# Kernel optimization log

Measured on AMD Instinct MI355X. Metric: run time of the kernel, lower is better.

Reference implementation:

```python
import jax, jax.numpy as jnp
import numpy as np

DIM = 768
HEADS = 12
HEAD_DIM = DIM // HEADS
GRID = 32
MLP_HIDDEN = DIM * 4
EPS = 1e-5


def layernorm(x, g, b):
    m = jnp.mean(x, axis=-1, keepdims=True)
    v = jnp.mean((x - m) ** 2, axis=-1, keepdims=True)
    return (x - m) * jax.lax.rsqrt(v + EPS) * g + b


def geometry_bias(wg_w, wg_b):
    # Box-relational embedding on a GRIDxGRID grid; batch-invariant so computed once.
    g = GRID
    idx = jnp.arange(g, dtype=jnp.float32)
    px = jnp.repeat(idx, g) / g          # row index, normalized
    py = jnp.tile(idx, g) / g            # col index, normalized
    cx = px + 0.5 / g
    cy = py + 0.5 / g
    wbox = 1.0 + 1.0 / g                 # x_max - x_min + 1 (constant)
    dx = jnp.log(jnp.clip(jnp.abs((cx[:, None] - cx[None, :]) / wbox), 1e-3, None))
    dy = jnp.log(jnp.clip(jnp.abs((cy[:, None] - cy[None, :]) / wbox), 1e-3, None))
    dz = jnp.zeros_like(dx)              # log(w/w) = log(h/h) = 0
    pos = jnp.stack([dx, dy, dz, dz], axis=-1)                      # [N,N,4]
    dim_mat = 1.0 / (1000.0 ** (jnp.arange(8, dtype=jnp.float32) / 8.0))
    mul = (100.0 * pos)[..., None] * dim_mat                        # [N,N,4,8]
    mul = mul.reshape(g * g, g * g, 32)
    emb = jnp.concatenate([jnp.sin(mul), jnp.cos(mul)], axis=-1)    # [N,N,64]
    w = jax.nn.relu(jnp.einsum('ijd,hd->hij', emb, wg_w) + wg_b[:, None, None])
    rgw = jnp.log(jnp.clip(w, 1e-6, None))                          # [H,N,N]
    return jnp.pad(rgw, ((0, 0), (1, 0), (1, 0)))                   # zero row/col for cls


def mha(x, qkv_w, proj_w, proj_b, bias=None):
    Bt, N, C = x.shape
    qkv = (x @ qkv_w.T).reshape(Bt, N, 3, HEADS, HEAD_DIM).transpose(2, 0, 3, 1, 4)
    q, k, v = qkv[0], qkv[1], qkv[2]
    attn = jnp.einsum('bhid,bhjd->bhij', q, k) * (HEAD_DIM ** -0.5)
    if bias is not None:
        attn = attn + bias
    attn = jax.nn.softmax(attn, axis=-1)
    out = jnp.einsum('bhij,bhjd->bhid', attn, v).transpose(0, 2, 1, 3).reshape(Bt, N, C)
    return out @ proj_w.T + proj_b


def mlp(x, fc1_w, fc1_b, fc2_w, fc2_b):
    h = jax.nn.gelu(x @ fc1_w.T + fc1_b, approximate=False)
    return h @ fc2_w.T + fc2_b


def setup_inputs() -> dict:
    key = jax.random.key(0)
    ks = jax.random.split(key, 16)
    s = 0.02
    d = {
        'x': jax.random.normal(ks[0], (2, 4097, DIM), dtype=jnp.float32),
        'norm1_g': jnp.ones((DIM,), jnp.float32), 'norm1_b': jnp.zeros((DIM,), jnp.float32),
        'qkv_w': s * jax.random.normal(ks[1], (3 * DIM, DIM), dtype=jnp.float32),
        'proj_w': s * jax.random.normal(ks[2], (DIM, DIM), dtype=jnp.float32),
        'proj_b': jnp.zeros((DIM,), jnp.float32),
        'wg_w': s * jax.random.normal(ks[3], (HEADS, 64), dtype=jnp.float32),
        'wg_b': s * jax.random.normal(ks[4], (HEADS,), dtype=jnp.float32),
        'tnorm1_g': jnp.ones((DIM,), jnp.float32), 'tnorm1_b': jnp.zeros((DIM,), jnp.float32),
        'tqkv_w': s * jax.random.normal(ks[5], (3 * DIM, DIM), dtype=jnp.float32),
        'tproj_w': s * jax.random.normal(ks[6], (DIM, DIM), dtype=jnp.float32),
        'tproj_b': jnp.zeros((DIM,), jnp.float32),
        'tfc_w': s * jax.random.normal(ks[7], (DIM, DIM), dtype=jnp.float32),
        'tfc_b': jnp.zeros((DIM,), jnp.float32),
        'norm2_g': jnp.ones((DIM,), jnp.float32), 'norm2_b': jnp.zeros((DIM,), jnp.float32),
        'fc1_w': s * jax.random.normal(ks[8], (MLP_HIDDEN, DIM), dtype=jnp.float32),
        'fc1_b': jnp.zeros((MLP_HIDDEN,), jnp.float32),
        'fc2_w': s * jax.random.normal(ks[9], (DIM, MLP_HIDDEN), dtype=jnp.float32),
        'fc2_b': jnp.zeros((DIM,), jnp.float32),
        'B': 2, 'T': 4, 'W': 32,
    }
    return d


def reference(x, norm1_g, norm1_b, qkv_w, proj_w, proj_b, wg_w, wg_b,
              tnorm1_g, tnorm1_b, tqkv_w, tproj_w, tproj_b, tfc_w, tfc_b,
              norm2_g, norm2_b, fc1_w, fc1_b, fc2_w, fc2_b, B, T, W):
    m = x.shape[2]
    H = ((x.shape[1] - 1) // T) // W
    # temporal attention: b (h w t) m -> (b h w) t m
    xt = x[:, 1:, :]
    xt_t = xt.reshape(B, H, W, T, m).reshape(B * H * W, T, m)
    res_t = mha(layernorm(xt_t, tnorm1_g, tnorm1_b), tqkv_w, tproj_w, tproj_b)
    res_t = res_t.reshape(B, H, W, T, m).reshape(B, H * W * T, m)
    res_t = res_t @ tfc_w.T + tfc_b
    xt = x[:, 1:, :] + res_t
    # spatial attention with geometric bias: b (h w t) m -> (b t) (h w) m
    init_cls = x[:, 0:1, :]
    cls = jnp.broadcast_to(init_cls, (B, T, m)).reshape(B * T, 1, m)
    xs = xt.reshape(B, H, W, T, m).transpose(0, 3, 1, 2, 4).reshape(B * T, H * W, m)
    xs = jnp.concatenate([cls, xs], axis=1)
    bias = geometry_bias(wg_w, wg_b)[None]  # [1,heads,1+HW,1+HW]
    res_s = mha(layernorm(xs, norm1_g, norm1_b), qkv_w, proj_w, proj_b, bias=bias)
    cls_out = res_s[:, 0, :].reshape(B, T, m).mean(axis=1, keepdims=True)
    res_s = res_s[:, 1:, :].reshape(B, T, H, W, m).transpose(0, 2, 3, 1, 4).reshape(B, H * W * T, m)
    xout = jnp.concatenate([init_cls, xt], axis=1) + jnp.concatenate([cls_out, res_s], axis=1)
    xout = xout + mlp(layernorm(xout, norm2_g, norm2_b), fc1_w, fc1_b, fc2_w, fc2_b)
    return xout
```

## Files before the change

### kernel.cpp

```cpp
#include <hip/hip_runtime.h>
#include <stdint.h>

#define DIM   768
#define HEADS 12
#define NSP   1025
#define VT_LD 1152
#define PS_LD 72

typedef __attribute__((ext_vector_type(8))) short short8;
typedef __attribute__((ext_vector_type(4))) float f32x4;
typedef unsigned short u16;
typedef unsigned int   u32;

__device__ __forceinline__ u16 f2bf(float v) {
  u32 u = __builtin_bit_cast(u32, v);
  u += 0x7fffu + ((u >> 16) & 1u);
  return (u16)(u >> 16);
}
__device__ __forceinline__ float bf2f(u16 h) {
  u32 u = ((u32)h) << 16;
  return __builtin_bit_cast(float, u);
}

__device__ __forceinline__ void load_lds16(const u16* g, u16* lbase, int lane) {
#if __has_builtin(__builtin_amdgcn_global_load_lds)
  __builtin_amdgcn_global_load_lds((const __attribute__((address_space(1))) void*)g,
                                   (__attribute__((address_space(3))) void*)lbase, 16, 0, 0);
#else
  *(short8*)(lbase + lane * 8) = *(const short8*)g;
#endif
}

__global__ __launch_bounds__(256) void zero_k(float* __restrict__ o, long n) {
  long i = (long)blockIdx.x * 256 + threadIdx.x;
  if (i < n) o[i] = 0.0f;
}

__global__ __launch_bounds__(256) void cvt_k(const float* __restrict__ src,
                                             u16* __restrict__ dst, long n) {
  long i = (long)blockIdx.x * 256 + threadIdx.x;
  if (i < n) dst[i] = f2bf(src[i]);
}

__device__ __forceinline__ void ln_row(const float* __restrict__ src,
                                       u16* __restrict__ dst,
                                       const float* __restrict__ g,
                                       const float* __restrict__ b) {
  int tid = threadIdx.x;
  float v[3];
  float s = 0.f, ss = 0.f;
#pragma unroll
  for (int i = 0; i < 3; i++) {
    v[i] = src[tid + i * 256];
    s += v[i];
    ss += v[i] * v[i];
  }
  __shared__ float red[8];
#pragma unroll
  for (int m = 32; m; m >>= 1) {
    s  += __shfl_xor(s, m);
    ss += __shfl_xor(ss, m);
  }
  int wid = tid >> 6;
  if ((tid & 63) == 0) { red[wid] = s; red[4 + wid] = ss; }
  __syncthreads();
  s  = red[0] + red[1] + red[2] + red[3];
  ss = red[4] + red[5] + red[6] + red[7];
  float mean = s * (1.0f / 768.0f);
  float var  = ss * (1.0f / 768.0f) - mean * mean;
  float rs = rsqrtf(var + 1e-5f);
#pragma unroll
  for (int i = 0; i < 3; i++) {
    int c = tid + i * 256;
    dst[c] = f2bf((v[i] - mean) * rs * g[c] + b[c]);
  }
}

__global__ __launch_bounds__(256) void ln_xt_k(const float* __restrict__ x,
                                               const float* __restrict__ g,
                                               const float* __restrict__ b,
                                               u16* __restrict__ outb) {
  int q = blockIdx.x, bb = blockIdx.y;
  const float* src = x + ((long)bb * 4097 + 1 + q) * DIM;
  u16* dst = outb + ((long)bb * 4096 + q) * DIM;
  ln_row(src, dst, g, b);
}

__global__ __launch_bounds__(256) void ln_xs_k(const float* __restrict__ x,
                                               const float* __restrict__ xt,
                                               const float* __restrict__ g,
                                               const float* __restrict__ b,
                                               u16* __restrict__ outb) {
  int n = blockIdx.x, bt = blockIdx.y;
  int bb = bt >> 2, t = bt & 3;
  const float* src;
  if (n == 0) src = x + (long)bb * 4097 * DIM;
  else        src = xt + ((long)bb * 4096 + (long)(n - 1) * 4 + t) * DIM;
  u16* dst = outb + ((long)bt * NSP + n) * DIM;
  ln_row(src, dst, g, b);
}

struct GemmParams {
  const u16* A; long lda, sA1;
  const u16* B; long ldb;
  void* C;      long ldc, sC1;
  const float* bias;
  const float* resid; long ldr, sR1;
  float scale;
  int M, N, K;
};

template <bool OUTBF16, bool BIASV, bool RESID, bool GELU_, bool NT64>
__global__ __launch_bounds__(256) void gemm_k(GemmParams p) {
  constexpr int NJ = NT64 ? 2 : 4;
  __shared__ u16 As[4096];
  __shared__ u16 Bs[NT64 ? 2048 : 4096];
  int tid = threadIdx.x;
  int z1 = blockIdx.z;
  const u16* A = p.A + (long)z1 * p.sA1;
  const u16* B = p.B;
  int m0 = blockIdx.y * 128, n0 = blockIdx.x * (NT64 ? 64 : 128);
  int wave = tid >> 6, lane = tid & 63;
  int quad = lane >> 4, lrow = lane & 15;
  int wm = (wave & 1) * 64;
  int wn = NT64 ? (wave >> 1) * 32 : (wave >> 1) * 64;

  int rA0 = m0 + (tid >> 2);        if (rA0 > p.M - 1) rA0 = p.M - 1;
  int rA1 = m0 + 64 + (tid >> 2);   if (rA1 > p.M - 1) rA1 = p.M - 1;
  int c8 = (tid & 3) << 3;
  const u16* pa0 = A + (long)rA0 * p.lda + c8;
  const u16* pa1 = A + (long)rA1 * p.lda + c8;
  u16* lA0 = As + wave * 512;  u16* lA1 = As + 2048 + wave * 512;

  const u16 *pb0, *pb1 = nullptr;
  u16 *lB0, *lB1 = nullptr;
  {
    int rB0 = n0 + (tid >> 2);
    if (!NT64) {
      int rB1 = n0 + 64 + (tid >> 2);
      if (rB0 > p.N - 1) rB0 = p.N - 1;
      if (rB1 > p.N - 1) rB1 = p.N - 1;
      pb1 = B + (long)rB1 * p.ldb + c8;
      lB1 = Bs + 2048 + wave * 512;
    }
    pb0 = B + (long)rB0 * p.ldb + c8;
    lB0 = Bs + wave * 512;
  }

  f32x4 acc[4][NJ];
#pragma unroll
  for (int i = 0; i < 4; i++)
#pragma unroll
    for (int j = 0; j < NJ; j++) acc[i][j] = (f32x4){0.f, 0.f, 0.f, 0.f};

  for (int k0 = 0; k0 < p.K; k0 += 32) {
    load_lds16(pa0 + k0, lA0, lane);
    load_lds16(pa1 + k0, lA1, lane);
    load_lds16(pb0 + k0, lB0, lane);
    if (!NT64) load_lds16(pb1 + k0, lB1, lane);
    __syncthreads();
    short8 af[4], bfr[NJ];
#pragma unroll
    for (int i = 0; i < 4; i++)  af[i]  = *(const short8*)&As[(wm + i * 16 + lrow) * 32 + quad * 8];
#pragma unroll
    for (int j = 0; j < NJ; j++) bfr[j] = *(const short8*)&Bs[(wn + j * 16 + lrow) * 32 + quad * 8];
#pragma unroll
    for (int i = 0; i < 4; i++)
#pragma unroll
      for (int j = 0; j < NJ; j++)
        acc[i][j] = __builtin_amdgcn_mfma_f32_16x16x32_bf16(af[i], bfr[j], acc[i][j], 0, 0, 0);
    __syncthreads();
  }

  float* Cf = (float*)p.C;
  u16*   Ch = (u16*)p.C;
  long cbase = (long)z1 * p.sC1;
#pragma unroll
  for (int i = 0; i < 4; i++) {
    int rbase = m0 + wm + i * 16 + quad * 4;
#pragma unroll
    for (int j = 0; j < NJ; j++) {
      int c = n0 + wn + j * 16 + lrow;
      if (c >= p.N) continue;
#pragma unroll
      for (int rr = 0; rr < 4; rr++) {
        int r = rbase + rr;
        if (r >= p.M) continue;
        float v = acc[i][j][rr] * p.scale;
        if (BIASV) v += p.bias[c];
        if (GELU_) v = 0.5f * v * (1.0f + erff(v * 0.70710678118654752f));
        if (RESID) v += p.resid[(long)z1 * p.sR1 + (long)r * p.ldr + c];
        long o = cbase + (long)r * p.ldc + c;
        if (OUTBF16) Ch[o] = f2bf(v);
        else         Cf[o] = v;
      }
    }
  }
}

__global__ __launch_bounds__(64) void attn_t_k(const u16* __restrict__ qkv,
                                               u16* __restrict__ outb) {
  int h = blockIdx.x;
  int g = blockIdx.y;
  int d = threadIdx.x;
  long base = (long)g * 4 * 2304 + h * 64 + d;
  float q[4], k[4], vv[4];
#pragma unroll
  for (int t = 0; t < 4; t++) {
    q[t]  = bf2f(qkv[base + (long)t * 2304]);
    k[t]  = bf2f(qkv[base + (long)t * 2304 + 768]);
    vv[t] = bf2f(qkv[base + (long)t * 2304 + 1536]);
  }
  float sc[4][4];
#pragma unroll
  for (int i = 0; i < 4; i++)
#pragma unroll
    for (int j = 0; j < 4; j++) {
      float pv = q[i] * k[j];
#pragma unroll
      for (int m = 32; m; m >>= 1) pv += __shfl_xor(pv, m);
      sc[i][j] = pv * 0.125f;
    }
#pragma unroll
  for (int i = 0; i < 4; i++) {
    float mx = fmaxf(fmaxf(sc[i][0], sc[i][1]), fmaxf(sc[i][2], sc[i][3]));
    float e0 = __expf(sc[i][0] - mx), e1 = __expf(sc[i][1] - mx);
    float e2 = __expf(sc[i][2] - mx), e3 = __expf(sc[i][3] - mx);
    float inv = 1.0f / (e0 + e1 + e2 + e3);
    float ov = (e0 * vv[0] + e1 * vv[1] + e2 * vv[2] + e3 * vv[3]) * inv;
    outb[((long)g * 4 + i) * DIM + h * 64 + d] = f2bf(ov);
  }
}

__global__ void geo_pre_k(const float* __restrict__ wg_w,
                          const float* __restrict__ wg_b,
                          float* __restrict__ sxsyc) {
  int t = threadIdx.x;
  if (t >= 384) return;
  int h = t >> 5, dd = t & 31;
  float dx = logf(fmaxf((float)dd * (1.0f / 33.0f), 0.001f));
  float sx = 0.f, sy = 0.f;
#pragma unroll
  for (int k2 = 0; k2 < 8; k2++) {
    float dm = powf(1000.0f, -(float)k2 / 8.0f);
    float a = 100.0f * dx * dm;
    float sn = sinf(a), cs = cosf(a);
    sx += sn * wg_w[h * 64 + k2]     + cs * wg_w[h * 64 + 32 + k2];
    sy += sn * wg_w[h * 64 + 8 + k2] + cs * wg_w[h * 64 + 40 + k2];
  }
  sxsyc[t] = sx;
  sxsyc[384 + t] = sy;
  if (dd == 0) {
    float c = wg_b[h];
#pragma unroll
    for (int k2 = 48; k2 < 64; k2++) c += wg_w[h * 64 + k2];
    sxsyc[768 + h] = c;
  }
}

__global__ __launch_bounds__(256) void geo_bias_k(const float* __restrict__ sxsyc,
                                                  float* __restrict__ Bh_g) {
  int h = blockIdx.x / 4;
  int idx = (blockIdx.x % 4) * 256 + threadIdx.x;
  int dr = idx >> 5, dc = idx & 31;
  float v = sxsyc[h * 32 + dr] + sxsyc[384 + h * 32 + dc] + sxsyc[768 + h];
  Bh_g[h * 1024 + idx] = logf(fmaxf(fmaxf(v, 0.0f), 1e-6f));
}

__global__ __launch_bounds__(256) void vtrans_k(const u16* __restrict__ qkv_s,
                                                u16* __restrict__ Vt) {
  __shared__ u16 tile[64][33];
  int bh = blockIdx.y;
  int bt = bh / 12, h = bh % 12;
  int j0 = blockIdx.x * 32;
  int tid = threadIdx.x;
#pragma unroll
  for (int it = 0; it < 8; it++) {
    int jj = it * 4 + (tid >> 6);
    int d = tid & 63;
    int j = j0 + jj;
    u16 v = 0;
    if (j < NSP) v = qkv_s[((long)bt * NSP + j) * 2304 + 1536 + h * 64 + d];
    tile[d][jj] = v;
  }
  __syncthreads();
#pragma unroll
  for (int it = 0; it < 8; it++) {
    int d = it * 8 + (tid >> 5);
    int j = tid & 31;
    Vt[((long)bh * 64 + d) * VT_LD + j0 + j] = tile[d][j];
  }
}

__global__ __launch_bounds__(256, 4) void attn_s_k(const u16* __restrict__ qkv,
                                                   const u16* __restrict__ Vt,
                                                   const float* __restrict__ Bh_g,
                                                   u16* __restrict__ attn_o) {
  __shared__ u16 KsF[8192];
  __shared__ u16 UN[4608];
  __shared__ float BhS[1024];
  const int bid = blockIdx.x;
  const int slot = bid >> 3;
  const int bh = (bid & 7) * 12 + slot / 17;
  const int qt = slot % 17;
  const int bt = bh / 12, h = bh % 12;
  const int tid = threadIdx.x;
  const int wave = tid >> 6, lane = tid & 63;
  const int quad = lane >> 4, lr = lane & 15;
  const int m0 = qt * 64;
  const long qb = (long)bt * NSP * 2304 + h * 64;

#pragma unroll
  for (int i = 0; i < 4; i++) BhS[tid + i * 256] = Bh_g[h * 1024 + tid + i * 256];

  const int rowq = tid >> 2, colq = (tid & 3) << 3;
  {
    int tokq = m0 + rowq; if (tokq > 1024) tokq = 1024;
    const u16* gq = qkv + qb + (long)tokq * 2304 + colq;
    load_lds16(gq,      UN + wave * 512, lane);
    load_lds16(gq + 32, UN + 2048 + wave * 512, lane);
  }
  {
    int t0 = rowq; if (t0 > 1024) t0 = 1024;
    const u16* g0 = qkv + qb + 768 + (long)t0 * 2304 + colq;
    load_lds16(g0,      KsF + wave * 512, lane);
    load_lds16(g0 + 32, KsF + 2048 + wave * 512, lane);
  }
  __syncthreads();
  short8 qf[2];
#pragma unroll
  for (int ks = 0; ks < 2; ks++)
    qf[ks] = *(const short8*)&UN[ks * 2048 + (wave * 16 + lr) * 32 + quad * 8];

  f32x4 Oa[4];
  float mr[4], lsum[4];
#pragma unroll
  for (int n = 0; n < 4; n++) Oa[n] = (f32x4){0.f, 0.f, 0.f, 0.f};
#pragma unroll
  for (int r = 0; r < 4; r++) { mr[r] = -1e30f; lsum[r] = 0.f; }

  int rid[4], ri_[4], ci_[4];
  float rok[4];
#pragma unroll
  for (int r = 0; r < 4; r++) {
    int i0 = m0 + wave * 16 + quad * 4 + r;
    rid[r] = i0;
    int ii = i0 < NSP ? i0 : (NSP - 1);
    int im1 = ii > 0 ? ii - 1 : 0;
    ri_[r] = im1 >> 5;
    ci_[r] = im1 & 31;
    rok[r] = (i0 > 0) ? 1.0f : 0.0f;
  }

  const u16* vrow = Vt + ((long)bh * 64 + lr) * VT_LD;

  for (int kt = 0; kt < 17; kt++) {
    const int cur = kt & 1, nxt = cur ^ 1;
    if (kt < 16) {
      int t0 = (kt + 1) * 64 + rowq; if (t0 > 1024) t0 = 1024;
      const u16* g0 = qkv + qb + 768 + (long)t0 * 2304 + colq;
      load_lds16(g0,      KsF + nxt * 4096 + wave * 512, lane);
      load_lds16(g0 + 32, KsF + nxt * 4096 + 2048 + wave * 512, lane);
    }
    short8 vf0[4], vf1[4];
#pragma unroll
    for (int n = 0; n < 4; n++)
      vf0[n] = *(const short8*)(vrow + (long)n * 16 * VT_LD + kt * 64 + quad * 8);
    f32x4 sa[4];
#pragma unroll
    for (int j = 0; j < 4; j++) sa[j] = (f32x4){0.f, 0.f, 0.f, 0.f};
#pragma unroll
    for (int ks = 0; ks < 2; ks++) {
#pragma unroll
      for (int j = 0; j < 4; j++) {
        short8 kf = *(const short8*)&KsF[cur * 4096 + ks * 2048 + (j * 16 + lr) * 32 + quad * 8];
        sa[j] = __builtin_amdgcn_mfma_f32_16x16x32_bf16(qf[ks], kf, sa[j], 0, 0, 0);
      }
    }
#pragma unroll
    for (int n = 0; n < 4; n++)
      vf1[n] = *(const short8*)(vrow + (long)n * 16 * VT_LD + kt * 64 + 32 + quad * 8);
#pragma unroll
    for (int j = 0; j < 4; j++) {
      int j0 = kt * 64 + j * 16 + lr;
      bool jv = j0 < NSP;
      int jm1 = j0 > 0 ? j0 - 1 : 0;
      if (jm1 > 1023) jm1 = 1023;
      int rj = jm1 >> 5, cj = jm1 & 31;
      float jnz = (j0 > 0) ? 1.0f : 0.0f;
#pragma unroll
      for (int r = 0; r < 4; r++) {
        int ad = ri_[r] - rj; ad = ad < 0 ? -ad : ad;
        int cd = ci_[r] - cj; cd = cd < 0 ? -cd : cd;
        float sv = sa[j][r] * 0.125f + BhS[ad * 32 + cd] * jnz * rok[r];
        sa[j][r] = jv ? sv : -1e30f;
      }
    }
    float alpha[4];
#pragma unroll
    for (int r = 0; r < 4; r++) {
      float tm = fmaxf(fmaxf(sa[0][r], sa[1][r]), fmaxf(sa[2][r], sa[3][r]));
      tm = fmaxf(tm, __shfl_xor(tm, 1));
      tm = fmaxf(tm, __shfl_xor(tm, 2));
      tm = fmaxf(tm, __shfl_xor(tm, 4));
      tm = fmaxf(tm, __shfl_xor(tm, 8));
      float mn = fmaxf(mr[r], tm);
      float a = __expf(mr[r] - mn);
      alpha[r] = a;
      float ls = 0.f;
      int prow = (wave * 16 + quad * 4 + r) * PS_LD;
#pragma unroll
      for (int j = 0; j < 4; j++) {
        float pp = __expf(sa[j][r] - mn);
        ls += pp;
        UN[prow + j * 16 + lr] = f2bf(pp);
      }
      lsum[r] = lsum[r] * a + ls;
      mr[r] = mn;
    }
#pragma unroll
    for (int n = 0; n < 4; n++)
#pragma unroll
      for (int r = 0; r < 4; r++) Oa[n][r] *= alpha[r];
#pragma unroll
    for (int ks = 0; ks < 2; ks++) {
      short8 pf = *(const short8*)&UN[(wave * 16 + lr) * PS_LD + ks * 32 + quad * 8];
#pragma unroll
      for (int n = 0; n < 4; n++)
        Oa[n] = __builtin_amdgcn_mfma_f32_16x16x32_bf16(pf, ks ? vf1[n] : vf0[n], Oa[n], 0, 0, 0);
    }
    __syncthreads();
  }
#pragma unroll
  for (int r = 0; r < 4; r++) {
    float l = lsum[r];
    l += __shfl_xor(l, 1);
    l += __shfl_xor(l, 2);
    l += __shfl_xor(l, 4);
    l += __shfl_xor(l, 8);
    lsum[r] = 1.0f / l;
  }
#pragma unroll
  for (int r = 0; r < 4; r++) {
    int i0 = rid[r];
    if (i0 < NSP) {
      long ob = ((long)bt * NSP + i0) * 768 + h * 64;
#pragma unroll
      for (int n = 0; n < 4; n++)
        attn_o[ob + n * 16 + lr] = f2bf(Oa[n][r] * lsum[r]);
    }
  }
}

__global__ __launch_bounds__(256) void assemble_ln_k(const float* __restrict__ x,
                                                     const float* __restrict__ xt,
                                                     const float* __restrict__ res_s,
                                                     const float* __restrict__ g,
                                                     const float* __restrict__ b,
                                                     float* __restrict__ outp,
                                                     u16* __restrict__ ln2b) {
  int n = blockIdx.x, bb = blockIdx.y;
  int tid = threadIdx.x;
  long ob = ((long)bb * 4097 + n) * DIM;
  float val[3];
  if (n == 0) {
#pragma unroll
    for (int i = 0; i < 3; i++) {
      int c = tid + i * 256;
      float acc = x[ob + c];
#pragma unroll
      for (int t = 0; t < 4; t++)
        acc += 0.25f * res_s[((long)(bb * 4 + t) * NSP) * DIM + c];
      val[i] = acc;
    }
  } else {
    int q = n - 1, hw = q >> 2, t = q & 3;
    long rs = ((long)(bb * 4 + t) * NSP + 1 + hw) * DIM;
    long xb = ((long)bb * 4096 + q) * DIM;
#pragma unroll
    for (int i = 0; i < 3; i++) {
      int c = tid + i * 256;
      val[i] = xt[xb + c] + res_s[rs + c];
    }
  }
  float s = 0.f, ss = 0.f;
#pragma unroll
  for (int i = 0; i < 3; i++) {
    outp[ob + tid + i * 256] = val[i];
    s += val[i];
    ss += val[i] * val[i];
  }
  __shared__ float red[8];
#pragma unroll
  for (int m = 32; m; m >>= 1) {
    s  += __shfl_xor(s, m);
    ss += __shfl_xor(ss, m);
  }
  int wid = tid >> 6;
  if ((tid & 63) == 0) { red[wid] = s; red[4 + wid] = ss; }
  __syncthreads();
  s  = red[0] + red[1] + red[2] + red[3];
  ss = red[4] + red[5] + red[6] + red[7];
  float mean = s * (1.0f / 768.0f);
  float var  = ss * (1.0f / 768.0f) - mean * mean;
  float rs = rsqrtf(var + 1e-5f);
#pragma unroll
  for (int i = 0; i < 3; i++) {
    int c = tid + i * 256;
    ln2b[ob + c] = f2bf((val[i] - mean) * rs * g[c] + b[c]);
  }
}

extern "C" void kernel_launch(void* const* d_in, const int* in_sizes, int n_in,
                              void* d_out, int out_size, void* d_ws, size_t ws_size,
                              hipStream_t stream) {
  const float* x        = (const float*)d_in[0];
  const float* norm1_g  = (const float*)d_in[1];
  const float* norm1_b  = (const float*)d_in[2];
  const float* qkv_w    = (const float*)d_in[3];
  const float* proj_w   = (const float*)d_in[4];
  const float* proj_b   = (const float*)d_in[5];
  const float* wg_w     = (const float*)d_in[6];
  const float* wg_b     = (const float*)d_in[7];
  const float* tnorm1_g = (const float*)d_in[8];
  const float* tnorm1_b = (const float*)d_in[9];
  const float* tqkv_w   = (const float*)d_in[10];
  const float* tproj_w  = (const float*)d_in[11];
  const float* tproj_b  = (const float*)d_in[12];
  const float* tfc_w    = (const float*)d_in[13];
  const float* tfc_b    = (const float*)d_in[14];
  const float* norm2_g  = (const float*)d_in[15];
  const float* norm2_b  = (const float*)d_in[16];
  const float* fc1_w    = (const float*)d_in[17];
  const float* fc1_b    = (const float*)d_in[18];
  const float* fc2_w    = (const float*)d_in[19];
  const float* fc2_b    = (const float*)d_in[20];
  float* out = (float*)d_out;
  (void)in_sizes; (void)n_in; (void)out_size;

  char* base = (char*)d_ws;
  size_t off = 0;
  auto take = [&](size_t bytes) -> char* {
    char* p = base + off;
    off += (bytes + 255) & ~(size_t)255;
    return p;
  };

  u16* wb_tqkv = (u16*)take(2304LL * 768 * 2);
  u16* wb_tprj = (u16*)take(768LL * 768 * 2);
  u16* wb_tfc  = (u16*)take(768LL * 768 * 2);
  u16* wb_qkv  = (u16*)take(2304LL * 768 * 2);
  u16* wb_proj = (u16*)take(768LL * 768 * 2);
  u16* wb_fc1  = (u16*)take(3072LL * 768 * 2);
  u16* wb_fc2  = (u16*)take(3072LL * 768 * 2);
  float* xt_f  = (float*)take(8192LL * 768 * 4);
  float* sxsyc = (float*)take(4096);
  float* Bh_g  = (float*)take(12LL * 1024 * 4);
  char* pool   = take(64536576);
  size_t REQ = off;

  u16* qkv_t  = (u16*)(pool);
  u16* ln_xt  = (u16*)(pool + 37748736);
  u16* attn_t = ln_xt;
  u16* h1     = (u16*)(pool + 50331648);
  u16* qkv_s  = (u16*)(pool);
  u16* ln_xs  = (u16*)(pool + 37785600);
  u16* attn_sp = ln_xs;
  u16* Vt     = (u16*)(pool + 50380800);
  u16* ln2b   = (u16*)(pool);
  float* res_s = (float*)(pool + 12585984);
  u16* geluh  = (u16*)(pool + 12585984);

  if (ws_size < REQ) {
    long n = 2LL * 4097 * 768;
    zero_k<<<dim3((n + 255) / 256), 256, 0, stream>>>(out, n);
    return;
  }

  {
    struct { const float* s; u16* d; long n; } cv[7] = {
      {tqkv_w, wb_tqkv, 2304LL * 768}, {tproj_w, wb_tprj, 768LL * 768},
      {tfc_w, wb_tfc, 768LL * 768},    {qkv_w, wb_qkv, 2304LL * 768},
      {proj_w, wb_proj, 768LL * 768},  {fc1_w, wb_fc1, 3072LL * 768},
      {fc2_w, wb_fc2, 3072LL * 768}};
    for (int i = 0; i < 7; i++)
      cvt_k<<<dim3((cv[i].n + 255) / 256), 256, 0, stream>>>(cv[i].s, cv[i].d, cv[i].n);
  }
  geo_pre_k<<<1, 384, 0, stream>>>(wg_w, wg_b, sxsyc);
  geo_bias_k<<<48, 256, 0, stream>>>(sxsyc, Bh_g);

  ln_xt_k<<<dim3(4096, 2), 256, 0, stream>>>(x, tnorm1_g, tnorm1_b, ln_xt);
  {
    GemmParams p{};
    p.A = ln_xt; p.lda = 768; p.B = wb_tqkv; p.ldb = 768;
    p.C = qkv_t; p.ldc = 2304; p.scale = 1.0f;
    p.M = 8192; p.N = 2304; p.K = 768;
    gemm_k<true, false, false, false, false><<<dim3(18, 64, 1), 256, 0, stream>>>(p);
  }
  attn_t_k<<<dim3(12, 2048), 64, 0, stream>>>(qkv_t, attn_t);
  {
    GemmParams p{};
    p.A = attn_t; p.lda = 768; p.B = wb_tprj; p.ldb = 768;
    p.C = h1; p.ldc = 768; p.bias = tproj_b; p.scale = 1.0f;
    p.M = 8192; p.N = 768; p.K = 768;
    gemm_k<true, true, false, false, true><<<dim3(12, 64, 1), 256, 0, stream>>>(p);
  }
  {
    GemmParams p{};
    p.A = h1; p.lda = 768; p.sA1 = 4096LL * 768;
    p.B = wb_tfc; p.ldb = 768;
    p.C = xt_f; p.ldc = 768; p.sC1 = 4096LL * 768;
    p.bias = tfc_b;
    p.resid = x + 768; p.ldr = 768; p.sR1 = 4097LL * 768;
    p.scale = 1.0f;
    p.M = 4096; p.N = 768; p.K = 768;
    gemm_k<false, true, true, false, true><<<dim3(12, 32, 2), 256, 0, stream>>>(p);
  }

  ln_xs_k<<<dim3(NSP, 8), 256, 0, stream>>>(x, xt_f, norm1_g, norm1_b, ln_xs);
  {
    GemmParams p{};
    p.A = ln_xs; p.lda = 768; p.B = wb_qkv; p.ldb = 768;
    p.C = qkv_s; p.ldc = 2304; p.scale = 1.0f;
    p.M = 8200; p.N = 2304; p.K = 768;
    gemm_k<true, false, false, false, false><<<dim3(18, 65, 1), 256, 0, stream>>>(p);
  }
  vtrans_k<<<dim3(36, 96), 256, 0, stream>>>(qkv_s, Vt);
  attn_s_k<<<dim3(1632), 256, 0, stream>>>(qkv_s, Vt, Bh_g, attn_sp);
  {
    GemmParams p{};
    p.A = attn_sp; p.lda = 768; p.B = wb_proj; p.ldb = 768;
    p.C = res_s; p.ldc = 768; p.bias = proj_b; p.scale = 1.0f;
    p.M = 8200; p.N = 768; p.K = 768;
    gemm_k<false, true, false, false, true><<<dim3(12, 65, 1), 256, 0, stream>>>(p);
  }
  assemble_ln_k<<<dim3(4097, 2), 256, 0, stream>>>(x, xt_f, res_s, norm2_g, norm2_b, out, ln2b);

  {
    GemmParams p{};
    p.A = ln2b; p.lda = 768; p.B = wb_fc1; p.ldb = 768;
    p.C = geluh; p.ldc = 3072; p.bias = fc1_b; p.scale = 1.0f;
    p.M = 8194; p.N = 3072; p.K = 768;
    gemm_k<true, true, false, true, false><<<dim3(24, 65, 1), 256, 0, stream>>>(p);
  }
  {
    GemmParams p{};
    p.A = geluh; p.lda = 3072; p.B = wb_fc2; p.ldb = 3072;
    p.C = out; p.ldc = 768; p.bias = fc2_b;
    p.resid = out; p.ldr = 768; p.scale = 1.0f;
    p.M = 8194; p.N = 768; p.K = 3072;
    gemm_k<false, true, true, false, true><<<dim3(12, 65, 1), 256, 0, stream>>>(p);
  }
}
```

Measured before the change: 744.9 us.

## Precompute bf16 bias in MFMA fragment layout and use exp2 softmax

```diff
diff --git a/kernel.cpp b/kernel.cpp
--- a/kernel.cpp
+++ b/kernel.cpp
@@ -8,9 +8,12 @@
 #define PS_LD 72
 
 typedef __attribute__((ext_vector_type(8))) short short8;
+typedef __attribute__((ext_vector_type(4))) short s16x4;
 typedef __attribute__((ext_vector_type(4))) float f32x4;
 typedef unsigned short u16;
 typedef unsigned int   u32;
+
+#define LOG2E 1.44269504088896f
 
 __device__ __forceinline__ u16 f2bf(float v) {
   u32 u = __builtin_bit_cast(u32, v);
@@ -21,6 +24,7 @@
   u32 u = ((u32)h) << 16;
   return __builtin_bit_cast(float, u);
 }
+__device__ __forceinline__ float bf2f_s(short h) { return bf2f((u16)h); }
 
 __device__ __forceinline__ void load_lds16(const u16* g, u16* lbase, int lane) {
 #if __has_builtin(__builtin_amdgcn_global_load_lds)
@@ -258,13 +262,36 @@
   }
 }
 
-__global__ __launch_bounds__(256) void geo_bias_k(const float* __restrict__ sxsyc,
-                                                  float* __restrict__ Bh_g) {
-  int h = blockIdx.x / 4;
-  int idx = (blockIdx.x % 4) * 256 + threadIdx.x;
-  int dr = idx >> 5, dc = idx & 31;
-  float v = sxsyc[h * 32 + dr] + sxsyc[384 + h * 32 + dc] + sxsyc[768 + h];
-  Bh_g[h * 1024 + idx] = logf(fmaxf(fmaxf(v, 0.0f), 1e-6f));
+__global__ __launch_bounds__(256) void bias_frag_k(const float* __restrict__ sxsyc,
+                                                   u16* __restrict__ Bf) {
+  int h = blockIdx.y;
+  int strip = blockIdx.x / 17, kt = blockIdx.x % 17;
+  int tid = threadIdx.x;
+  int quad = tid >> 6, lr = (tid >> 2) & 15, j = tid & 3;
+  int j0 = kt * 64 + j * 16 + lr;
+  int rj = 0, cj = 0;
+  bool jvalid = (j0 > 0 && j0 < NSP);
+  if (jvalid) { rj = (j0 - 1) >> 5; cj = (j0 - 1) & 31; }
+  float ch = sxsyc[768 + h];
+  s16x4 outv;
+#pragma unroll
+  for (int r = 0; r < 4; r++) {
+    int i0 = strip * 16 + quad * 4 + r;
+    float bv;
+    if (j0 >= NSP) bv = -1e30f;
+    else if (j0 == 0 || i0 == 0) bv = 0.0f;
+    else {
+      int im1 = i0 - 1; if (im1 > 1023) im1 = 1023;
+      int ri = im1 >> 5, ci = im1 & 31;
+      int ad = ri - rj; ad = ad < 0 ? -ad : ad;
+      int cd = ci - cj; cd = cd < 0 ? -cd : cd;
+      float v = sxsyc[h * 32 + ad] + sxsyc[384 + h * 32 + cd] + ch;
+      bv = logf(fmaxf(fmaxf(v, 0.0f), 1e-6f)) * LOG2E;
+    }
+    outv[r] = (short)f2bf(bv);
+  }
+  long ob = (((long)h * 68 + strip) * 17 + kt) * 1024 + (long)tid * 4;
+  *(s16x4*)(Bf + ob) = outv;
 }
 
 __global__ __launch_bounds__(256) void vtrans_k(const u16* __restrict__ qkv_s,
@@ -292,13 +319,12 @@
   }
 }
 
-__global__ __launch_bounds__(256, 4) void attn_s_k(const u16* __restrict__ qkv,
+__global__ __launch_bounds__(256, 6) void attn_s_k(const u16* __restrict__ qkv,
                                                    const u16* __restrict__ Vt,
-                                                   const float* __restrict__ Bh_g,
+                                                   const u16* __restrict__ Bf,
                                                    u16* __restrict__ attn_o) {
   __shared__ u16 KsF[8192];
   __shared__ u16 UN[4608];
-  __shared__ float BhS[1024];
   const int bid = blockIdx.x;
   const int slot = bid >> 3;
   const int bh = (bid & 7) * 12 + slot / 17;
@@ -310,9 +336,6 @@
   const int m0 = qt * 64;
   const long qb = (long)bt * NSP * 2304 + h * 64;
 
-#pragma unroll
-  for (int i = 0; i < 4; i++) BhS[tid + i * 256] = Bh_g[h * 1024 + tid + i * 256];
-
   const int rowq = tid >> 2, colq = (tid & 3) << 3;
   {
     int tokq = m0 + rowq; if (tokq > 1024) tokq = 1024;
@@ -339,20 +362,11 @@
 #pragma unroll
   for (int r = 0; r < 4; r++) { mr[r] = -1e30f; lsum[r] = 0.f; }
 
-  int rid[4], ri_[4], ci_[4];
-  float rok[4];
-#pragma unroll
-  for (int r = 0; r < 4; r++) {
-    int i0 = m0 + wave * 16 + quad * 4 + r;
-    rid[r] = i0;
-    int ii = i0 < NSP ? i0 : (NSP - 1);
-    int im1 = ii > 0 ? ii - 1 : 0;
-    ri_[r] = im1 >> 5;
-    ci_[r] = im1 & 31;
-    rok[r] = (i0 > 0) ? 1.0f : 0.0f;
-  }
-
   const u16* vrow = Vt + ((long)bh * 64 + lr) * VT_LD;
+  const u16* bfp = Bf + (((long)h * 68 + qt * 4 + wave) * 17) * 1024 + (long)lane * 16;
+  const int pwr = (wave * 16 + quad * 4) * PS_LD;
+  const int prd = (wave * 16 + lr) * PS_LD;
+  const int rkey = ((lr >> 2) & 3) * 16;
 
   for (int kt = 0; kt < 17; kt++) {
     const int cur = kt & 1, nxt = cur ^ 1;
@@ -362,6 +376,9 @@
       load_lds16(g0,      KsF + nxt * 4096 + wave * 512, lane);
       load_lds16(g0 + 32, KsF + nxt * 4096 + 2048 + wave * 512, lane);
     }
+    short8 bf0 = *(const short8*)(bfp);
+    short8 bf1 = *(const short8*)(bfp + 8);
+    bfp += 1024;
     short8 vf0[4], vf1[4];
 #pragma unroll
     for (int n = 0; n < 4; n++)
@@ -381,21 +398,12 @@
     for (int n = 0; n < 4; n++)
       vf1[n] = *(const short8*)(vrow + (long)n * 16 * VT_LD + kt * 64 + 32 + quad * 8);
 #pragma unroll
-    for (int j = 0; j < 4; j++) {
-      int j0 = kt * 64 + j * 16 + lr;
-      bool jv = j0 < NSP;
-      int jm1 = j0 > 0 ? j0 - 1 : 0;
-      if (jm1 > 1023) jm1 = 1023;
-      int rj = jm1 >> 5, cj = jm1 & 31;
-      float jnz = (j0 > 0) ? 1.0f : 0.0f;
+    for (int j = 0; j < 4; j++)
 #pragma unroll
       for (int r = 0; r < 4; r++) {
-        int ad = ri_[r] - rj; ad = ad < 0 ? -ad : ad;
-        int cd = ci_[r] - cj; cd = cd < 0 ? -cd : cd;
-        float sv = sa[j][r] * 0.125f + BhS[ad * 32 + cd] * jnz * rok[r];
-        sa[j][r] = jv ? sv : -1e30f;
+        float bias = (j < 2) ? bf2f_s(bf0[j * 4 + r]) : bf2f_s(bf1[(j - 2) * 4 + r]);
+        sa[j][r] = fmaf(sa[j][r], 0.125f * LOG2E, bias);
       }
-    }
     float alpha[4];
 #pragma unroll
     for (int r = 0; r < 4; r++) {
@@ -405,17 +413,16 @@
       tm = fmaxf(tm, __shfl_xor(tm, 4));
       tm = fmaxf(tm, __shfl_xor(tm, 8));
       float mn = fmaxf(mr[r], tm);
-      float a = __expf(mr[r] - mn);
-      alpha[r] = a;
+      alpha[r] = exp2f(mr[r] - mn);
       float ls = 0.f;
-      int prow = (wave * 16 + quad * 4 + r) * PS_LD;
+      int prow = pwr + r * PS_LD;
 #pragma unroll
       for (int j = 0; j < 4; j++) {
-        float pp = __expf(sa[j][r] - mn);
+        float pp = exp2f(sa[j][r] - mn);
         ls += pp;
-        UN[prow + j * 16 + lr] = f2bf(pp);
+        UN[prow + ((j ^ quad) * 16 + lr)] = f2bf(pp);
       }
-      lsum[r] = lsum[r] * a + ls;
+      lsum[r] = lsum[r] * alpha[r] + ls;
       mr[r] = mn;
     }
 #pragma unroll
@@ -424,7 +431,7 @@
       for (int r = 0; r < 4; r++) Oa[n][r] *= alpha[r];
 #pragma unroll
     for (int ks = 0; ks < 2; ks++) {
-      short8 pf = *(const short8*)&UN[(wave * 16 + lr) * PS_LD + ks * 32 + quad * 8];
+      short8 pf = *(const short8*)&UN[prd + (((ks * 32 + quad * 8) ^ rkey))];
 #pragma unroll
       for (int n = 0; n < 4; n++)
         Oa[n] = __builtin_amdgcn_mfma_f32_16x16x32_bf16(pf, ks ? vf1[n] : vf0[n], Oa[n], 0, 0, 0);
@@ -442,7 +449,7 @@
   }
 #pragma unroll
   for (int r = 0; r < 4; r++) {
-    int i0 = rid[r];
+    int i0 = m0 + wave * 16 + quad * 4 + r;
     if (i0 < NSP) {
       long ob = ((long)bt * NSP + i0) * 768 + h * 64;
 #pragma unroll
@@ -555,7 +562,7 @@
   u16* wb_fc2  = (u16*)take(3072LL * 768 * 2);
   float* xt_f  = (float*)take(8192LL * 768 * 4);
   float* sxsyc = (float*)take(4096);
-  float* Bh_g  = (float*)take(12LL * 1024 * 4);
+  u16* Bf      = (u16*)take(12LL * 68 * 17 * 1024 * 2);
   char* pool   = take(64536576);
   size_t REQ = off;
 
@@ -587,7 +594,7 @@
       cvt_k<<<dim3((cv[i].n + 255) / 256), 256, 0, stream>>>(cv[i].s, cv[i].d, cv[i].n);
   }
   geo_pre_k<<<1, 384, 0, stream>>>(wg_w, wg_b, sxsyc);
-  geo_bias_k<<<48, 256, 0, stream>>>(sxsyc, Bh_g);
+  bias_frag_k<<<dim3(68 * 17, 12), 256, 0, stream>>>(sxsyc, Bf);
 
   ln_xt_k<<<dim3(4096, 2), 256, 0, stream>>>(x, tnorm1_g, tnorm1_b, ln_xt);
   {
@@ -626,7 +633,7 @@
     gemm_k<true, false, false, false, false><<<dim3(18, 65, 1), 256, 0, stream>>>(p);
   }
   vtrans_k<<<dim3(36, 96), 256, 0, stream>>>(qkv_s, Vt);
-  attn_s_k<<<dim3(1632), 256, 0, stream>>>(qkv_s, Vt, Bh_g, attn_sp);
+  attn_s_k<<<dim3(1632), 256, 0, stream>>>(qkv_s, Vt, Bf, attn_sp);
   {
     GemmParams p{};
     p.A = attn_sp; p.lda = 768; p.B = wb_proj; p.ldb = 768;
```

After: 827.1 us. +11.0%, slower.
